# Kernel optimization log

Hardware: AMD Instinct MI355X
Metric: run time of the kernel (lower is better)

Reference implementation:

```python
import jax, jax.numpy as jnp
import numpy as np

B, H, W, C = 32, 128, 128, 128


def setup_inputs() -> dict:
    key = jax.random.key(0)
    k1, k2 = jax.random.split(key)
    x = jax.random.normal(k1, (B, H, W, C), dtype=jnp.float32)
    W_sel = jax.random.normal(k2, (C, 4), dtype=jnp.float32) * 0.05
    b_sel = jnp.zeros((4,), dtype=jnp.float32)
    return {"x": x, "W_sel": W_sel, "b_sel": b_sel}


def reference(x, W_sel, b_sel):
    # selector: softmax(Dense(mean over H,W))  -> [B, 4]
    pooled = jnp.mean(x, axis=(1, 2))                      # [B, C]
    weights = jax.nn.softmax(pooled @ W_sel + b_sel, axis=-1)  # [B, 4]
    # weighted sum of the 4 counter-clockwise 90-degree rotations
    # (tf.image.rot90 is CCW, matching jnp.rot90 with axes=(1, 2))
    out = jnp.zeros_like(x)
    for i in range(4):
        rot = jnp.rot90(x, k=i, axes=(1, 2))               # [B, H, W, C]
        out = out + rot * weights[:, i, None, None, None]
    return out
```

## Files before the change

### kernel.cpp

```cpp
#include <hip/hip_runtime.h>

#define HW    128
#define CDIM  128
#define BDIM  32
#define NPIX  (HW * HW)
#define N1    (HW - 1)
#define SLABS 64

typedef float vfloat4 __attribute__((ext_vector_type(4)));

__device__ __forceinline__ void nt_store4(float4* p, float4 v) {
    vfloat4 t;
    t.x = v.x; t.y = v.y; t.z = v.z; t.w = v.w;
    __builtin_nontemporal_store(t, (vfloat4*)p);
}

__global__ __launch_bounds__(256) void k1_partial(
    const float* __restrict__ x,
    const float* __restrict__ Wsel,
    float* __restrict__ partial) {
    int blk  = blockIdx.x;
    int b    = blk >> 6;
    int slab = blk & 63;
    int tid  = threadIdx.x;
    int c4   = tid & 31;
    int po   = tid >> 5;

    const float4* xb = (const float4*)(x + (size_t)b * NPIX * CDIM);
    float4 acc = make_float4(0.f, 0.f, 0.f, 0.f);
    int pixbase = slab * 256 + po;
    #pragma unroll 4
    for (int k = 0; k < 32; ++k) {
        int pix = pixbase + k * 8;
        float4 v = xb[(size_t)pix * 32 + c4];
        acc.x += v.x; acc.y += v.y; acc.z += v.z; acc.w += v.w;
    }

    const float4* W4 = (const float4*)Wsel;
    float4 w0 = W4[c4 * 4 + 0];
    float4 w1 = W4[c4 * 4 + 1];
    float4 w2 = W4[c4 * 4 + 2];
    float4 w3 = W4[c4 * 4 + 3];
    float4 lg;
    lg.x = acc.x * w0.x + acc.y * w1.x + acc.z * w2.x + acc.w * w3.x;
    lg.y = acc.x * w0.y + acc.y * w1.y + acc.z * w2.y + acc.w * w3.y;
    lg.z = acc.x * w0.z + acc.y * w1.z + acc.z * w2.z + acc.w * w3.z;
    lg.w = acc.x * w0.w + acc.y * w1.w + acc.z * w2.w + acc.w * w3.w;

    __shared__ float4 s[256];
    s[tid] = lg;
    __syncthreads();
    #pragma unroll
    for (int off = 128; off > 0; off >>= 1) {
        if (tid < off) {
            float4 a = s[tid], c = s[tid + off];
            a.x += c.x; a.y += c.y; a.z += c.z; a.w += c.w;
            s[tid] = a;
        }
        __syncthreads();
    }
    if (tid == 0) ((float4*)partial)[blk] = s[0];
}

__global__ __launch_bounds__(64) void k2_weights(
    const float* __restrict__ partial,
    const float* __restrict__ bsel,
    float* __restrict__ wts) {
    int b = blockIdx.x;
    int t = threadIdx.x;
    float4 v = ((const float4*)partial)[b * 64 + t];
    #pragma unroll
    for (int off = 32; off > 0; off >>= 1) {
        v.x += __shfl_down(v.x, off, 64);
        v.y += __shfl_down(v.y, off, 64);
        v.z += __shfl_down(v.z, off, 64);
        v.w += __shfl_down(v.w, off, 64);
    }
    if (t == 0) {
        const float inv = 1.0f / (float)NPIX;
        float l0 = v.x * inv + bsel[0];
        float l1 = v.y * inv + bsel[1];
        float l2 = v.z * inv + bsel[2];
        float l3 = v.w * inv + bsel[3];
        float m  = fmaxf(fmaxf(l0, l1), fmaxf(l2, l3));
        float e0 = expf(l0 - m), e1 = expf(l1 - m);
        float e2 = expf(l2 - m), e3 = expf(l3 - m);
        float inv_s = 1.0f / (e0 + e1 + e2 + e3);
        wts[b * 4 + 0] = e0 * inv_s;
        wts[b * 4 + 1] = e1 * inv_s;
        wts[b * 4 + 2] = e2 * inv_s;
        wts[b * 4 + 3] = e3 * inv_s;
    }
}

__device__ __forceinline__ float4 comb(float s0, float s1, float s2, float s3,
                                       float4 a, float4 b, float4 c, float4 d) {
    float4 r;
    r.x = s0 * a.x + s1 * b.x + s2 * c.x + s3 * d.x;
    r.y = s0 * a.y + s1 * b.y + s2 * c.y + s3 * d.y;
    r.z = s0 * a.z + s1 * b.z + s2 * c.z + s3 * d.z;
    r.w = s0 * a.w + s1 * b.w + s2 * c.w + s3 * d.w;
    return r;
}

__global__ __launch_bounds__(256) void k3_rot(
    const float* __restrict__ x,
    const float* __restrict__ wts,
    float* __restrict__ out) {
    int blk = blockIdx.x;
    int b   = blk >> 9;
    int grp = blk & 511;
    int tid = threadIdx.x;
    int c4  = tid & 31;
    int o   = tid >> 5;
    int orbit = grp * 8 + o;
    int h = orbit >> 6;
    int w = orbit & 63;

    float s0 = wts[b * 4 + 0];
    float s1 = wts[b * 4 + 1];
    float s2 = wts[b * 4 + 2];
    float s3 = wts[b * 4 + 3];

    const float4* xb = (const float4*)(x + (size_t)b * NPIX * CDIM);
    float4*       ob = (float4*)(out + (size_t)b * NPIX * CDIM);

    int p0 = (h * HW + w) * 32 + c4;
    int p1 = (w * HW + (N1 - h)) * 32 + c4;
    int p2 = ((N1 - h) * HW + (N1 - w)) * 32 + c4;
    int p3 = ((N1 - w) * HW + h) * 32 + c4;

    float4 a0 = xb[p0];
    float4 a1 = xb[p1];
    float4 a2 = xb[p2];
    float4 a3 = xb[p3];

    nt_store4(&ob[p0], comb(s0, s1, s2, s3, a0, a1, a2, a3));
    nt_store4(&ob[p1], comb(s0, s1, s2, s3, a1, a2, a3, a0));
    nt_store4(&ob[p2], comb(s0, s1, s2, s3, a2, a3, a0, a1));
    nt_store4(&ob[p3], comb(s0, s1, s2, s3, a3, a0, a1, a2));
}

extern "C" void kernel_launch(void* const* d_in, const int* in_sizes, int n_in,
                              void* d_out, int out_size, void* d_ws, size_t ws_size,
                              hipStream_t stream) {
    const float* x    = (const float*)d_in[0];
    const float* Wsel = (const float*)d_in[1];
    const float* bsel = (const float*)d_in[2];
    float* out = (float*)d_out;

    float* partial = (float*)d_ws;
    float* wts     = (float*)((char*)d_ws + 2048 * 4 * sizeof(float));

    k1_partial<<<BDIM * SLABS, 256, 0, stream>>>(x, Wsel, partial);
    k2_weights<<<BDIM, 64, 0, stream>>>(partial, bsel, wts);
    k3_rot<<<BDIM * 512, 256, 0, stream>>>(x, wts, out);
}
```

Baseline: 123.9 us.

## Stage a bf16 copy of x during pooling and read it in rotation kernel

The pooling kernel now also writes a bf16-rounded copy of x into workspace, using nontemporal loads. The rotation kernel reads that half-width copy instead of the fp32 input. The aim is to cut the bytes read by the bandwidth-bound rotation pass. The cost is an extra write pass in the first kernel, so total memory traffic stays about the same, and the output loses precision because inputs are rounded to bf16. A fallback to the original path runs if the workspace is too small.

Measured after the change: 137.5 us. 1.11x slower.

```diff
diff --git a/kernel.cpp b/kernel.cpp
--- a/kernel.cpp
+++ b/kernel.cpp
@@ -9,10 +9,89 @@
 
 typedef float vfloat4 __attribute__((ext_vector_type(4)));
 
+__device__ __forceinline__ float4 nt_load4(const float4* p) {
+    vfloat4 t = __builtin_nontemporal_load((const vfloat4*)p);
+    float4 r; r.x = t.x; r.y = t.y; r.z = t.z; r.w = t.w;
+    return r;
+}
+
 __device__ __forceinline__ void nt_store4(float4* p, float4 v) {
     vfloat4 t;
     t.x = v.x; t.y = v.y; t.z = v.z; t.w = v.w;
     __builtin_nontemporal_store(t, (vfloat4*)p);
+}
+
+__device__ __forceinline__ unsigned int bf16_rne(float f) {
+    unsigned int u = __float_as_uint(f);
+    return (u + 0x7FFFu + ((u >> 16) & 1u)) >> 16;
+}
+
+__device__ __forceinline__ uint2 pack_bf16x4(float4 v) {
+    uint2 r;
+    r.x = bf16_rne(v.x) | (bf16_rne(v.y) << 16);
+    r.y = bf16_rne(v.z) | (bf16_rne(v.w) << 16);
+    return r;
+}
+
+__device__ __forceinline__ float4 unpack_bf16x4(uint2 pk) {
+    float4 r;
+    r.x = __uint_as_float(pk.x << 16);
+    r.y = __uint_as_float(pk.x & 0xFFFF0000u);
+    r.z = __uint_as_float(pk.y << 16);
+    r.w = __uint_as_float(pk.y & 0xFFFF0000u);
+    return r;
+}
+
+__global__ __launch_bounds__(256) void k1_partial_cvt(
+    const float* __restrict__ x,
+    const float* __restrict__ Wsel,
+    float* __restrict__ partial,
+    uint2* __restrict__ xbf) {
+    int blk  = blockIdx.x;
+    int b    = blk >> 6;
+    int slab = blk & 63;
+    int tid  = threadIdx.x;
+    int c4   = tid & 31;
+    int po   = tid >> 5;
+
+    size_t base4 = (size_t)b * NPIX * 32;
+    const float4* xb  = (const float4*)x + base4;
+    uint2*        bfb = xbf + base4;
+
+    float4 acc = make_float4(0.f, 0.f, 0.f, 0.f);
+    int pixbase = slab * 256 + po;
+    #pragma unroll 4
+    for (int k = 0; k < 32; ++k) {
+        size_t idx = (size_t)(pixbase + k * 8) * 32 + c4;
+        float4 v = nt_load4(&xb[idx]);
+        acc.x += v.x; acc.y += v.y; acc.z += v.z; acc.w += v.w;
+        bfb[idx] = pack_bf16x4(v);
+    }
+
+    const float4* W4 = (const float4*)Wsel;
+    float4 w0 = W4[c4 * 4 + 0];
+    float4 w1 = W4[c4 * 4 + 1];
+    float4 w2 = W4[c4 * 4 + 2];
+    float4 w3 = W4[c4 * 4 + 3];
+    float4 lg;
+    lg.x = acc.x * w0.x + acc.y * w1.x + acc.z * w2.x + acc.w * w3.x;
+    lg.y = acc.x * w0.y + acc.y * w1.y + acc.z * w2.y + acc.w * w3.y;
+    lg.z = acc.x * w0.z + acc.y * w1.z + acc.z * w2.z + acc.w * w3.z;
+    lg.w = acc.x * w0.w + acc.y * w1.w + acc.z * w2.w + acc.w * w3.w;
+
+    __shared__ float4 s[256];
+    s[tid] = lg;
+    __syncthreads();
+    #pragma unroll
+    for (int off = 128; off > 0; off >>= 1) {
+        if (tid < off) {
+            float4 a = s[tid], c = s[tid + off];
+            a.x += c.x; a.y += c.y; a.z += c.z; a.w += c.w;
+            s[tid] = a;
+        }
+        __syncthreads();
+    }
+    if (tid == 0) ((float4*)partial)[blk] = s[0];
 }
 
 __global__ __launch_bounds__(256) void k1_partial(
@@ -35,7 +114,6 @@
         float4 v = xb[(size_t)pix * 32 + c4];
         acc.x += v.x; acc.y += v.y; acc.z += v.z; acc.w += v.w;
     }
-
     const float4* W4 = (const float4*)Wsel;
     float4 w0 = W4[c4 * 4 + 0];
     float4 w1 = W4[c4 * 4 + 1];
@@ -103,6 +181,45 @@
     return r;
 }
 
+__global__ __launch_bounds__(256) void k3_rot_bf(
+    const uint2* __restrict__ xbf,
+    const float* __restrict__ wts,
+    float* __restrict__ out) {
+    int blk = blockIdx.x;
+    int b   = blk >> 9;
+    int grp = blk & 511;
+    int tid = threadIdx.x;
+    int c4  = tid & 31;
+    int o   = tid >> 5;
+    int orbit = grp * 8 + o;
+    int h = orbit >> 6;
+    int w = orbit & 63;
+
+    float s0 = wts[b * 4 + 0];
+    float s1 = wts[b * 4 + 1];
+    float s2 = wts[b * 4 + 2];
+    float s3 = wts[b * 4 + 3];
+
+    size_t base4 = (size_t)b * NPIX * 32;
+    const uint2* xb = xbf + base4;
+    float4*      ob = (float4*)out + base4;
+
+    int p0 = (h * HW + w) * 32 + c4;
+    int p1 = (w * HW + (N1 - h)) * 32 + c4;
+    int p2 = ((N1 - h) * HW + (N1 - w)) * 32 + c4;
+    int p3 = ((N1 - w) * HW + h) * 32 + c4;
+
+    float4 a0 = unpack_bf16x4(xb[p0]);
+    float4 a1 = unpack_bf16x4(xb[p1]);
+    float4 a2 = unpack_bf16x4(xb[p2]);
+    float4 a3 = unpack_bf16x4(xb[p3]);
+
+    nt_store4(&ob[p0], comb(s0, s1, s2, s3, a0, a1, a2, a3));
+    nt_store4(&ob[p1], comb(s0, s1, s2, s3, a1, a2, a3, a0));
+    nt_store4(&ob[p2], comb(s0, s1, s2, s3, a2, a3, a0, a1));
+    nt_store4(&ob[p3], comb(s0, s1, s2, s3, a3, a0, a1, a2));
+}
+
 __global__ __launch_bounds__(256) void k3_rot(
     const float* __restrict__ x,
     const float* __restrict__ wts,
@@ -151,8 +268,17 @@
 
     float* partial = (float*)d_ws;
     float* wts     = (float*)((char*)d_ws + 2048 * 4 * sizeof(float));
-
-    k1_partial<<<BDIM * SLABS, 256, 0, stream>>>(x, Wsel, partial);
-    k2_weights<<<BDIM, 64, 0, stream>>>(partial, bsel, wts);
-    k3_rot<<<BDIM * 512, 256, 0, stream>>>(x, wts, out);
-}
+    uint2* xbf     = (uint2*)((char*)d_ws + 65536);
+
+    const size_t need = 65536 + (size_t)BDIM * NPIX * CDIM * 2;
+
+    if (ws_size >= need) {
+        k1_partial_cvt<<<BDIM * SLABS, 256, 0, stream>>>(x, Wsel, partial, xbf);
+        k2_weights<<<BDIM, 64, 0, stream>>>(partial, bsel, wts);
+        k3_rot_bf<<<BDIM * 512, 256, 0, stream>>>(xbf, wts, out);
+    } else {
+        k1_partial<<<BDIM * SLABS, 256, 0, stream>>>(x, Wsel, partial);
+        k2_weights<<<BDIM, 64, 0, stream>>>(partial, bsel, wts);
+        k3_rot<<<BDIM * 512, 256, 0, stream>>>(x, wts, out);
+    }
+}
```

## Fuse pooling, softmax and rotation into one persistent kernel with grid barrier

Applied to the files above, without the earlier changes.

Replaces three kernels with one persistent kernel that reads each input tile once. It accumulates the channel means, publishes per-block partials and spins on a global counter until every block has arrived. The loaded pixels are kept on chip as bf16 in LDS and registers, then redistributed through an LDS tile to write all four rotated outputs. This removes the second full read of x, but depends on all blocks being co-resident and lowers the precision of the stored intermediates.

Result: slower. 304.2 us (+145.5%).

```diff
diff --git a/kernel.cpp b/kernel.cpp
--- a/kernel.cpp
+++ b/kernel.cpp
@@ -1,144 +1,246 @@
 #include <hip/hip_runtime.h>
 
 #define HW    128
-#define CDIM  128
-#define BDIM  32
 #define NPIX  (HW * HW)
-#define N1    (HW - 1)
-#define SLABS 64
+#define NLDS  15
+#define NREG  49
 
 typedef float vfloat4 __attribute__((ext_vector_type(4)));
 
+__device__ __forceinline__ float4 nt_load4(const float4* p) {
+    vfloat4 t = __builtin_nontemporal_load((const vfloat4*)p);
+    return make_float4(t.x, t.y, t.z, t.w);
+}
 __device__ __forceinline__ void nt_store4(float4* p, float4 v) {
-    vfloat4 t;
-    t.x = v.x; t.y = v.y; t.z = v.z; t.w = v.w;
+    vfloat4 t; t.x = v.x; t.y = v.y; t.z = v.z; t.w = v.w;
     __builtin_nontemporal_store(t, (vfloat4*)p);
 }
 
-__global__ __launch_bounds__(256) void k1_partial(
-    const float* __restrict__ x,
-    const float* __restrict__ Wsel,
-    float* __restrict__ partial) {
-    int blk  = blockIdx.x;
-    int b    = blk >> 6;
-    int slab = blk & 63;
-    int tid  = threadIdx.x;
-    int c4   = tid & 31;
-    int po   = tid >> 5;
-
-    const float4* xb = (const float4*)(x + (size_t)b * NPIX * CDIM);
-    float4 acc = make_float4(0.f, 0.f, 0.f, 0.f);
-    int pixbase = slab * 256 + po;
-    #pragma unroll 4
-    for (int k = 0; k < 32; ++k) {
-        int pix = pixbase + k * 8;
-        float4 v = xb[(size_t)pix * 32 + c4];
-        acc.x += v.x; acc.y += v.y; acc.z += v.z; acc.w += v.w;
-    }
+__device__ __forceinline__ unsigned bf16_rne(float f) {
+    unsigned u = __float_as_uint(f);
+    return (u + 0x7FFFu + ((u >> 16) & 1u)) >> 16;
+}
+__device__ __forceinline__ unsigned pack2(float a, float b) {
+    return bf16_rne(a) | (bf16_rne(b) << 16);
+}
+__device__ __forceinline__ float unlo(unsigned u) { return __uint_as_float(u << 16); }
+__device__ __forceinline__ float unhi(unsigned u) { return __uint_as_float(u & 0xFFFF0000u); }
+
+__device__ __forceinline__ void unpack8(uint4 u, float (&a)[8]) {
+    a[0] = unlo(u.x); a[1] = unhi(u.x); a[2] = unlo(u.y); a[3] = unhi(u.y);
+    a[4] = unlo(u.z); a[5] = unhi(u.z); a[6] = unlo(u.w); a[7] = unhi(u.w);
+}
+
+__device__ __forceinline__ void store_comb(
+    float4* __restrict__ ob, int pix, int q,
+    float s0, float s1, float s2, float s3,
+    const float (&a)[8], const float (&b)[8], const float (&c)[8], const float (&d)[8]) {
+    float4 lo, hi;
+    lo.x = s0*a[0] + s1*b[0] + s2*c[0] + s3*d[0];
+    lo.y = s0*a[1] + s1*b[1] + s2*c[1] + s3*d[1];
+    lo.z = s0*a[2] + s1*b[2] + s2*c[2] + s3*d[2];
+    lo.w = s0*a[3] + s1*b[3] + s2*c[3] + s3*d[3];
+    hi.x = s0*a[4] + s1*b[4] + s2*c[4] + s3*d[4];
+    hi.y = s0*a[5] + s1*b[5] + s2*c[5] + s3*d[5];
+    hi.z = s0*a[6] + s1*b[6] + s2*c[6] + s3*d[6];
+    hi.w = s0*a[7] + s1*b[7] + s2*c[7] + s3*d[7];
+    size_t idx = (size_t)pix * 32 + q * 2;
+    nt_store4(&ob[idx],     lo);
+    nt_store4(&ob[idx + 1], hi);
+}
+
+#define GETPX(i) ((i) < NLDS ? perLDSv[t * NLDS + (i)] \
+    : make_uint4(rg[(i) - NLDS][0], rg[(i) - NLDS][1], rg[(i) - NLDS][2], rg[(i) - NLDS][3]))
+
+template <int BK>
+__device__ __forceinline__ void phaseA(
+    const float4* __restrict__ xb, int h0, int s, int q, int t,
+    uint4* __restrict__ perLDSv, unsigned (&rg)[NREG][4],
+    float4& acc0, float4& acc1) {
+    #pragma unroll
+    for (int i = 0; i < 64; ++i) {
+        int p;
+        if constexpr (BK == 0)      p = (h0 + s) * HW + i;
+        else if constexpr (BK == 1) p = (s * 8 + (i >> 3)) * HW + (120 - h0) + (i & 7);
+        else if constexpr (BK == 2) p = (120 - h0 + s) * HW + 64 + i;
+        else                        p = (64 + s * 8 + (i >> 3)) * HW + h0 + (i & 7);
+        const float4* src = xb + ((size_t)p * 32 + q * 2);
+        float4 v0 = nt_load4(src);
+        float4 v1 = nt_load4(src + 1);
+        acc0.x += v0.x; acc0.y += v0.y; acc0.z += v0.z; acc0.w += v0.w;
+        acc1.x += v1.x; acc1.y += v1.y; acc1.z += v1.z; acc1.w += v1.w;
+        uint4 d = make_uint4(pack2(v0.x, v0.y), pack2(v0.z, v0.w),
+                             pack2(v1.x, v1.y), pack2(v1.z, v1.w));
+        if (i < NLDS) {
+            perLDSv[t * NLDS + i] = d;
+        } else {
+            rg[i - NLDS][0] = d.x; rg[i - NLDS][1] = d.y;
+            rg[i - NLDS][2] = d.z; rg[i - NLDS][3] = d.w;
+        }
+    }
+}
+
+template <int DH, int HALF>
+__device__ __forceinline__ void tile_step(
+    int bk, int s, int q, int t, int h0,
+    const uint4* __restrict__ perLDSv, const unsigned (&rg)[NREG][4],
+    uint4* __restrict__ tilev,
+    float s0, float s1, float s2, float s3,
+    float4* __restrict__ ob) {
+    constexpr int W0 = HALF * 32;
+    if (bk == 0) {
+        if (s == DH) {
+            #pragma unroll
+            for (int i = W0; i < W0 + 32; ++i)
+                tilev[(0 * 32 + (i - W0)) * 16 + q] = GETPX(i);
+        }
+    } else if (bk == 1) {
+        if ((s >> 2) == HALF) {
+            #pragma unroll
+            for (int ii = 0; ii < 8; ++ii) {
+                int i  = ii * 8 + (7 - DH);
+                int ww = s * 8 + ii - W0;
+                tilev[(1 * 32 + ww) * 16 + q] = GETPX(i);
+            }
+        }
+    } else if (bk == 2) {
+        if (s == 7 - DH) {
+            #pragma unroll
+            for (int i = 32 - W0; i <= 63 - W0; ++i) {
+                int ww = 63 - i - W0;
+                tilev[(2 * 32 + ww) * 16 + q] = GETPX(i);
+            }
+        }
+    } else {
+        if ((s >> 2) == 1 - HALF) {
+            #pragma unroll
+            for (int ii = 0; ii < 8; ++ii) {
+                int i  = ii * 8 + DH;
+                int ww = 63 - s * 8 - ii - W0;
+                tilev[(3 * 32 + ww) * 16 + q] = GETPX(i);
+            }
+        }
+    }
+    __syncthreads();
+    {
+        int ww = t >> 4;
+        int w  = W0 + ww;
+        int h  = h0 + DH;
+        uint4 u0 = tilev[(0 * 32 + ww) * 16 + q];
+        uint4 u1 = tilev[(1 * 32 + ww) * 16 + q];
+        uint4 u2 = tilev[(2 * 32 + ww) * 16 + q];
+        uint4 u3 = tilev[(3 * 32 + ww) * 16 + q];
+        float a0[8], a1[8], a2[8], a3[8];
+        unpack8(u0, a0); unpack8(u1, a1); unpack8(u2, a2); unpack8(u3, a3);
+        int p0 = h * HW + w;
+        int p1 = w * HW + (127 - h);
+        int p2 = (127 - h) * HW + (127 - w);
+        int p3 = (127 - w) * HW + h;
+        store_comb(ob, p0, q, s0, s1, s2, s3, a0, a1, a2, a3);
+        store_comb(ob, p1, q, s0, s1, s2, s3, a1, a2, a3, a0);
+        store_comb(ob, p2, q, s0, s1, s2, s3, a2, a3, a0, a1);
+        store_comb(ob, p3, q, s0, s1, s2, s3, a3, a0, a1, a2);
+    }
+    __syncthreads();
+}
+
+__global__ __launch_bounds__(512, 2) void fused_rot(
+    const float* __restrict__ x, const float* __restrict__ Wsel,
+    const float* __restrict__ bsel, float* __restrict__ out,
+    float* __restrict__ partial, unsigned* __restrict__ cnt) {
+    __shared__ uint4 perLDSv[512 * NLDS];
+    __shared__ uint4 tilev[4 * 32 * 16];
+    __shared__ float wts_s[4];
+
+    const int t    = threadIdx.x;
+    const int q    = t & 15;
+    const int pg   = t >> 4;
+    const int bk   = pg >> 3;
+    const int s    = pg & 7;
+    const int wgid = blockIdx.x;
+    const int b    = wgid >> 3;
+    const int h0   = (wgid & 7) << 3;
+
+    const float4* xb = (const float4*)x + (size_t)b * NPIX * 32;
+    float4*       ob = (float4*)out + (size_t)b * NPIX * 32;
+
+    unsigned rg[NREG][4];
+    float4 acc0 = make_float4(0.f, 0.f, 0.f, 0.f);
+    float4 acc1 = make_float4(0.f, 0.f, 0.f, 0.f);
+
+    if (bk == 0)      phaseA<0>(xb, h0, s, q, t, perLDSv, rg, acc0, acc1);
+    else if (bk == 1) phaseA<1>(xb, h0, s, q, t, perLDSv, rg, acc0, acc1);
+    else if (bk == 2) phaseA<2>(xb, h0, s, q, t, perLDSv, rg, acc0, acc1);
+    else              phaseA<3>(xb, h0, s, q, t, perLDSv, rg, acc0, acc1);
 
     const float4* W4 = (const float4*)Wsel;
-    float4 w0 = W4[c4 * 4 + 0];
-    float4 w1 = W4[c4 * 4 + 1];
-    float4 w2 = W4[c4 * 4 + 2];
-    float4 w3 = W4[c4 * 4 + 3];
-    float4 lg;
-    lg.x = acc.x * w0.x + acc.y * w1.x + acc.z * w2.x + acc.w * w3.x;
-    lg.y = acc.x * w0.y + acc.y * w1.y + acc.z * w2.y + acc.w * w3.y;
-    lg.z = acc.x * w0.z + acc.y * w1.z + acc.z * w2.z + acc.w * w3.z;
-    lg.w = acc.x * w0.w + acc.y * w1.w + acc.z * w2.w + acc.w * w3.w;
-
-    __shared__ float4 s[256];
-    s[tid] = lg;
+    float4 lg = make_float4(0.f, 0.f, 0.f, 0.f);
+    {
+        float av[8] = {acc0.x, acc0.y, acc0.z, acc0.w,
+                       acc1.x, acc1.y, acc1.z, acc1.w};
+        #pragma unroll
+        for (int j = 0; j < 8; ++j) {
+            float4 wr = W4[q * 8 + j];
+            lg.x += av[j] * wr.x; lg.y += av[j] * wr.y;
+            lg.z += av[j] * wr.z; lg.w += av[j] * wr.w;
+        }
+    }
+    float4* red = (float4*)tilev;
+    red[t] = lg;
     __syncthreads();
     #pragma unroll
-    for (int off = 128; off > 0; off >>= 1) {
-        if (tid < off) {
-            float4 a = s[tid], c = s[tid + off];
+    for (int off = 256; off > 0; off >>= 1) {
+        if (t < off) {
+            float4 a = red[t], c = red[t + off];
             a.x += c.x; a.y += c.y; a.z += c.z; a.w += c.w;
-            s[tid] = a;
+            red[t] = a;
         }
         __syncthreads();
     }
-    if (tid == 0) ((float4*)partial)[blk] = s[0];
-}
-
-__global__ __launch_bounds__(64) void k2_weights(
-    const float* __restrict__ partial,
-    const float* __restrict__ bsel,
-    float* __restrict__ wts) {
-    int b = blockIdx.x;
-    int t = threadIdx.x;
-    float4 v = ((const float4*)partial)[b * 64 + t];
-    #pragma unroll
-    for (int off = 32; off > 0; off >>= 1) {
-        v.x += __shfl_down(v.x, off, 64);
-        v.y += __shfl_down(v.y, off, 64);
-        v.z += __shfl_down(v.z, off, 64);
-        v.w += __shfl_down(v.w, off, 64);
-    }
+
     if (t == 0) {
+        float4 r = red[0];
+        __hip_atomic_store(&partial[wgid * 4 + 0], r.x, __ATOMIC_RELAXED, __HIP_MEMORY_SCOPE_AGENT);
+        __hip_atomic_store(&partial[wgid * 4 + 1], r.y, __ATOMIC_RELAXED, __HIP_MEMORY_SCOPE_AGENT);
+        __hip_atomic_store(&partial[wgid * 4 + 2], r.z, __ATOMIC_RELAXED, __HIP_MEMORY_SCOPE_AGENT);
+        __hip_atomic_store(&partial[wgid * 4 + 3], r.w, __ATOMIC_RELAXED, __HIP_MEMORY_SCOPE_AGENT);
+        __hip_atomic_fetch_add(cnt, 1u, __ATOMIC_ACQ_REL, __HIP_MEMORY_SCOPE_AGENT);
+        while (__hip_atomic_load(cnt, __ATOMIC_ACQUIRE, __HIP_MEMORY_SCOPE_AGENT) < 256u)
+            __builtin_amdgcn_s_sleep(2);
+        float l[4] = {bsel[0], bsel[1], bsel[2], bsel[3]};
         const float inv = 1.0f / (float)NPIX;
-        float l0 = v.x * inv + bsel[0];
-        float l1 = v.y * inv + bsel[1];
-        float l2 = v.z * inv + bsel[2];
-        float l3 = v.w * inv + bsel[3];
-        float m  = fmaxf(fmaxf(l0, l1), fmaxf(l2, l3));
-        float e0 = expf(l0 - m), e1 = expf(l1 - m);
-        float e2 = expf(l2 - m), e3 = expf(l3 - m);
-        float inv_s = 1.0f / (e0 + e1 + e2 + e3);
-        wts[b * 4 + 0] = e0 * inv_s;
-        wts[b * 4 + 1] = e1 * inv_s;
-        wts[b * 4 + 2] = e2 * inv_s;
-        wts[b * 4 + 3] = e3 * inv_s;
-    }
-}
-
-__device__ __forceinline__ float4 comb(float s0, float s1, float s2, float s3,
-                                       float4 a, float4 b, float4 c, float4 d) {
-    float4 r;
-    r.x = s0 * a.x + s1 * b.x + s2 * c.x + s3 * d.x;
-    r.y = s0 * a.y + s1 * b.y + s2 * c.y + s3 * d.y;
-    r.z = s0 * a.z + s1 * b.z + s2 * c.z + s3 * d.z;
-    r.w = s0 * a.w + s1 * b.w + s2 * c.w + s3 * d.w;
-    return r;
-}
-
-__global__ __launch_bounds__(256) void k3_rot(
-    const float* __restrict__ x,
-    const float* __restrict__ wts,
-    float* __restrict__ out) {
-    int blk = blockIdx.x;
-    int b   = blk >> 9;
-    int grp = blk & 511;
-    int tid = threadIdx.x;
-    int c4  = tid & 31;
-    int o   = tid >> 5;
-    int orbit = grp * 8 + o;
-    int h = orbit >> 6;
-    int w = orbit & 63;
-
-    float s0 = wts[b * 4 + 0];
-    float s1 = wts[b * 4 + 1];
-    float s2 = wts[b * 4 + 2];
-    float s3 = wts[b * 4 + 3];
-
-    const float4* xb = (const float4*)(x + (size_t)b * NPIX * CDIM);
-    float4*       ob = (float4*)(out + (size_t)b * NPIX * CDIM);
-
-    int p0 = (h * HW + w) * 32 + c4;
-    int p1 = (w * HW + (N1 - h)) * 32 + c4;
-    int p2 = ((N1 - h) * HW + (N1 - w)) * 32 + c4;
-    int p3 = ((N1 - w) * HW + h) * 32 + c4;
-
-    float4 a0 = xb[p0];
-    float4 a1 = xb[p1];
-    float4 a2 = xb[p2];
-    float4 a3 = xb[p3];
-
-    nt_store4(&ob[p0], comb(s0, s1, s2, s3, a0, a1, a2, a3));
-    nt_store4(&ob[p1], comb(s0, s1, s2, s3, a1, a2, a3, a0));
-    nt_store4(&ob[p2], comb(s0, s1, s2, s3, a2, a3, a0, a1));
-    nt_store4(&ob[p3], comb(s0, s1, s2, s3, a3, a0, a1, a2));
+        for (int g = 0; g < 8; ++g) {
+            #pragma unroll
+            for (int k = 0; k < 4; ++k)
+                l[k] += __hip_atomic_load(&partial[(b * 8 + g) * 4 + k],
+                                          __ATOMIC_RELAXED, __HIP_MEMORY_SCOPE_AGENT) * inv;
+        }
+        float m  = fmaxf(fmaxf(l[0], l[1]), fmaxf(l[2], l[3]));
+        float e0 = expf(l[0] - m), e1 = expf(l[1] - m);
+        float e2 = expf(l[2] - m), e3 = expf(l[3] - m);
+        float is = 1.0f / (e0 + e1 + e2 + e3);
+        wts_s[0] = e0 * is; wts_s[1] = e1 * is;
+        wts_s[2] = e2 * is; wts_s[3] = e3 * is;
+    }
+    __syncthreads();
+    const float s0 = wts_s[0], s1 = wts_s[1], s2 = wts_s[2], s3 = wts_s[3];
+
+    tile_step<0, 0>(bk, s, q, t, h0, perLDSv, rg, tilev, s0, s1, s2, s3, ob);
+    tile_step<0, 1>(bk, s, q, t, h0, perLDSv, rg, tilev, s0, s1, s2, s3, ob);
+    tile_step<1, 0>(bk, s, q, t, h0, perLDSv, rg, tilev, s0, s1, s2, s3, ob);
+    tile_step<1, 1>(bk, s, q, t, h0, perLDSv, rg, tilev, s0, s1, s2, s3, ob);
+    tile_step<2, 0>(bk, s, q, t, h0, perLDSv, rg, tilev, s0, s1, s2, s3, ob);
+    tile_step<2, 1>(bk, s, q, t, h0, perLDSv, rg, tilev, s0, s1, s2, s3, ob);
+    tile_step<3, 0>(bk, s, q, t, h0, perLDSv, rg, tilev, s0, s1, s2, s3, ob);
+    tile_step<3, 1>(bk, s, q, t, h0, perLDSv, rg, tilev, s0, s1, s2, s3, ob);
+    tile_step<4, 0>(bk, s, q, t, h0, perLDSv, rg, tilev, s0, s1, s2, s3, ob);
+    tile_step<4, 1>(bk, s, q, t, h0, perLDSv, rg, tilev, s0, s1, s2, s3, ob);
+    tile_step<5, 0>(bk, s, q, t, h0, perLDSv, rg, tilev, s0, s1, s2, s3, ob);
+    tile_step<5, 1>(bk, s, q, t, h0, perLDSv, rg, tilev, s0, s1, s2, s3, ob);
+    tile_step<6, 0>(bk, s, q, t, h0, perLDSv, rg, tilev, s0, s1, s2, s3, ob);
+    tile_step<6, 1>(bk, s, q, t, h0, perLDSv, rg, tilev, s0, s1, s2, s3, ob);
+    tile_step<7, 0>(bk, s, q, t, h0, perLDSv, rg, tilev, s0, s1, s2, s3, ob);
+    tile_step<7, 1>(bk, s, q, t, h0, perLDSv, rg, tilev, s0, s1, s2, s3, ob);
 }
 
 extern "C" void kernel_launch(void* const* d_in, const int* in_sizes, int n_in,
@@ -149,10 +251,9 @@
     const float* bsel = (const float*)d_in[2];
     float* out = (float*)d_out;
 
-    float* partial = (float*)d_ws;
-    float* wts     = (float*)((char*)d_ws + 2048 * 4 * sizeof(float));
-
-    k1_partial<<<BDIM * SLABS, 256, 0, stream>>>(x, Wsel, partial);
-    k2_weights<<<BDIM, 64, 0, stream>>>(partial, bsel, wts);
-    k3_rot<<<BDIM * 512, 256, 0, stream>>>(x, wts, out);
-}
+    float*    partial = (float*)d_ws;
+    unsigned* cnt     = (unsigned*)((char*)d_ws + 4096);
+
+    hipMemsetAsync(cnt, 0, sizeof(unsigned), stream);
+    fused_rot<<<256, 512, 0, stream>>>(x, Wsel, bsel, out, partial, cnt);
+}
```
